# Kernel optimization log

Measured on AMD Instinct MI355X. Metric: run time of the kernel, lower is better.

The kernel has to match this reference:

```python
import jax, jax.numpy as jnp
import numpy as np

B, L, H, NH = 4, 200, 256, 4
HS = H // NH
NEG = jnp.float32(-(2.0**32) + 1.0)


def setup_inputs() -> dict:
    key = jax.random.key(0)
    ks = jax.random.split(key, 12)
    f = lambda k, s, sc=1.0: jax.random.normal(k, s, dtype=jnp.float32) * sc
    w_sc = 1.0 / np.sqrt(H).astype(np.float32)
    return {
        "queries": f(ks[0], (B, L, H)),
        "keys": f(ks[1], (B, L, H)),
        "time_matrix_K": f(ks[2], (B, L, L, H)),
        "time_matrix_V": f(ks[3], (B, L, L, H)),
        "dis_matrix_K": f(ks[4], (B, L, L, H)),
        "dis_matrix_V": f(ks[5], (B, L, L, H)),
        "abs_pos_K": f(ks[6], (B, L, H)),
        "abs_pos_V": f(ks[7], (B, L, H)),
        "Qw": f(ks[8], (H, H), w_sc),
        "Qb": jnp.zeros((H,), jnp.float32),
        "Kw": f(ks[9], (H, H), w_sc),
        "Kb": jnp.zeros((H,), jnp.float32),
        "Vw": f(ks[10], (H, H), w_sc),
        "Vb": jnp.zeros((H,), jnp.float32),
        "time_mask": jnp.zeros((B, L), dtype=bool),          # no padding positions
        "attn_mask": ~jnp.tril(jnp.ones((L, L), dtype=bool)),  # causal: mask strict upper triangle
    }


def reference(queries, keys, time_matrix_K, time_matrix_V, dis_matrix_K, dis_matrix_V,
              abs_pos_K, abs_pos_V, Qw, Qb, Kw, Kb, Vw, Vb, time_mask, attn_mask):
    # Linear projections (torch nn.Linear: x @ W^T + b)
    Q = queries @ Qw.T + Qb
    K = keys @ Kw.T + Kb
    V = keys @ Vw.T + Vb
    # split heads: [B, L, NH, HS]
    qh = Q.reshape(B, L, NH, HS)
    kh = K.reshape(B, L, NH, HS)
    vh = V.reshape(B, L, NH, HS)
    pKh = abs_pos_K.reshape(B, L, NH, HS)
    pVh = abs_pos_V.reshape(B, L, NH, HS)
    tKh = time_matrix_K.reshape(B, L, L, NH, HS)
    tVh = time_matrix_V.reshape(B, L, L, NH, HS)
    dKh = dis_matrix_K.reshape(B, L, L, NH, HS)
    dVh = dis_matrix_V.reshape(B, L, L, NH, HS)

    # attention logits [B, NH, L(query), L(key)] with three extra bias terms
    w = jnp.einsum("blhd,bmhd->bhlm", qh, kh)
    w += jnp.einsum("blhd,bmhd->bhlm", qh, pKh)
    w += jnp.einsum("blmhd,blhd->bhlm", tKh, qh)
    w += jnp.einsum("blmhd,blhd->bhlm", dKh, qh)
    w = w / jnp.sqrt(jnp.float32(HS))

    mask = time_mask[:, None, :, None] | attn_mask[None, None, :, :]
    w = jnp.where(mask, NEG, w)
    a = jax.nn.softmax(w, axis=-1)  # dropout_rate = 0 (eval)

    out = jnp.einsum("bhlm,bmhd->blhd", a, vh)
    out += jnp.einsum("bhlm,bmhd->blhd", a, pVh)
    out += jnp.einsum("bhlm,blmhd->blhd", a, tVh)
    out += jnp.einsum("bhlm,blmhd->blhd", a, dVh)
    return out.reshape(B, L, H)
```

## Files before the change

kernel.cpp:

```cpp
#include <hip/hip_runtime.h>
#include <cstddef>


#define B 4
#define L 200
#define H 256
#define NH 4
#define HS 64
#define SCALE 0.125f
#define NROWS 8

__global__ __launch_bounds__(256) void depoi_proj(
    const float* __restrict__ queries, const float* __restrict__ keys,
    const float* __restrict__ Qw, const float* __restrict__ Qb,
    const float* __restrict__ Kw, const float* __restrict__ Kb,
    const float* __restrict__ Vw, const float* __restrict__ Vb,
    const float* __restrict__ apK, const float* __restrict__ apV,
    float* __restrict__ Qo, float* __restrict__ Ko, float* __restrict__ Vo)
{
    __shared__ float4 xq[NROWS][H / 4];
    __shared__ float4 xk[NROWS][H / 4];
    const int t  = threadIdx.x;
    const int n0 = blockIdx.x * NROWS;

    const float4* q4 = (const float4*)queries;
    const float4* k4 = (const float4*)keys;
#pragma unroll
    for (int p = 0; p < (NROWS * (H / 4)) / 256; ++p) {
        int idx = p * 256 + t;
        int r = idx >> 6, c = idx & 63;
        xq[r][c] = q4[(size_t)(n0 + r) * (H / 4) + c];
        xk[r][c] = k4[(size_t)(n0 + r) * (H / 4) + c];
    }
    __syncthreads();

    float accq[NROWS], acck[NROWS], accv[NROWS];
#pragma unroll
    for (int r = 0; r < NROWS; ++r) { accq[r] = 0.f; acck[r] = 0.f; accv[r] = 0.f; }

    const float4* Qw4 = (const float4*)Qw + (size_t)t * (H / 4);
    const float4* Kw4 = (const float4*)Kw + (size_t)t * (H / 4);
    const float4* Vw4 = (const float4*)Vw + (size_t)t * (H / 4);
    for (int i = 0; i < H / 4; ++i) {
        float4 wq = Qw4[i], wk = Kw4[i], wv = Vw4[i];
#pragma unroll
        for (int r = 0; r < NROWS; ++r) {
            float4 a = xq[r][i];
            float4 c = xk[r][i];
            accq[r] += a.x * wq.x + a.y * wq.y + a.z * wq.z + a.w * wq.w;
            acck[r] += c.x * wk.x + c.y * wk.y + c.z * wk.z + c.w * wk.w;
            accv[r] += c.x * wv.x + c.y * wv.y + c.z * wv.z + c.w * wv.w;
        }
    }

    const float bq = Qb[t], bk = Kb[t], bv = Vb[t];
#pragma unroll
    for (int r = 0; r < NROWS; ++r) {
        size_t o = (size_t)(n0 + r) * H + t;
        Qo[o] = accq[r] + bq;
        Ko[o] = acck[r] + bk + apK[o];
        Vo[o] = accv[r] + bv + apV[o];
    }
}

__global__ __launch_bounds__(256) void depoi_attn(
    const float* __restrict__ Q, const float* __restrict__ Ksum,
    const float* __restrict__ Vsum,
    const float* __restrict__ tK, const float* __restrict__ dK,
    const float* __restrict__ tV, const float* __restrict__ dV,
    float* __restrict__ out)
{
    const int l = blockIdx.x;
    const int h = blockIdx.y;
    const int b = blockIdx.z;
    const int t    = threadIdx.x;
    const int mg   = t >> 4;
    const int dq   = t & 15;
    const int wid  = t >> 6;
    const int lane = t & 63;
    const int M = l + 1;

    __shared__ float4 sq[16];
    __shared__ float  plog[256];
    __shared__ float  sred[4];
    __shared__ float4 wpart[4][16];

    if (t < 16)
        sq[t] = ((const float4*)Q)[(size_t)(b * L + l) * (H / 4) + h * 16 + t];
    __syncthreads();
    const float4 q4 = sq[dq];

    const float4* K4  = (const float4*)Ksum;
    const float4* T4  = (const float4*)tK;
    const float4* D4  = (const float4*)dK;
    const size_t rowbase = (size_t)(b * L + l) * L * (H / 4);
    const size_t kbase   = (size_t)b * L * (H / 4);
    const int    col     = h * 16 + dq;

    for (int m = mg; m < M; m += 16) {
        float4 kk = K4[kbase + (size_t)m * (H / 4) + col];
        float4 tk = T4[rowbase + (size_t)m * (H / 4) + col];
        float4 dk = D4[rowbase + (size_t)m * (H / 4) + col];
        float sx = kk.x + tk.x + dk.x;
        float sy = kk.y + tk.y + dk.y;
        float sz = kk.z + tk.z + dk.z;
        float sw = kk.w + tk.w + dk.w;
        float p = q4.x * sx + q4.y * sy + q4.z * sz + q4.w * sw;
        p += __shfl_xor(p, 1);
        p += __shfl_xor(p, 2);
        p += __shfl_xor(p, 4);
        p += __shfl_xor(p, 8);
        if (dq == 0) plog[m] = p * SCALE;
    }
    __syncthreads();

    float v = (t < M) ? plog[t] : -3.0e38f;
    float mx = v;
#pragma unroll
    for (int off = 32; off >= 1; off >>= 1) mx = fmaxf(mx, __shfl_xor(mx, off));
    if (lane == 0) sred[wid] = mx;
    __syncthreads();
    mx = fmaxf(fmaxf(sred[0], sred[1]), fmaxf(sred[2], sred[3]));

    float p = (t < M) ? __expf(v - mx) : 0.0f;
    plog[t] = p;
    float s = p;
#pragma unroll
    for (int off = 32; off >= 1; off >>= 1) s += __shfl_xor(s, off);
    __syncthreads();
    if (lane == 0) sred[wid] = s;
    __syncthreads();
    const float inv = 1.0f / (sred[0] + sred[1] + sred[2] + sred[3]);

    const float4* V4  = (const float4*)Vsum;
    const float4* TV4 = (const float4*)tV;
    const float4* DV4 = (const float4*)dV;
    float4 acc = make_float4(0.f, 0.f, 0.f, 0.f);
    for (int m = mg; m < M; m += 16) {
        float pm = plog[m];
        float4 vv = V4[kbase + (size_t)m * (H / 4) + col];
        float4 tv = TV4[rowbase + (size_t)m * (H / 4) + col];
        float4 dv = DV4[rowbase + (size_t)m * (H / 4) + col];
        acc.x += pm * (vv.x + tv.x + dv.x);
        acc.y += pm * (vv.y + tv.y + dv.y);
        acc.z += pm * (vv.z + tv.z + dv.z);
        acc.w += pm * (vv.w + tv.w + dv.w);
    }
    acc.x += __shfl_xor(acc.x, 16); acc.y += __shfl_xor(acc.y, 16);
    acc.z += __shfl_xor(acc.z, 16); acc.w += __shfl_xor(acc.w, 16);
    acc.x += __shfl_xor(acc.x, 32); acc.y += __shfl_xor(acc.y, 32);
    acc.z += __shfl_xor(acc.z, 32); acc.w += __shfl_xor(acc.w, 32);
    if (lane < 16) wpart[wid][lane] = acc;
    __syncthreads();
    if (t < 16) {
        float4 a0 = wpart[0][t], a1 = wpart[1][t], a2 = wpart[2][t], a3 = wpart[3][t];
        float4 o;
        o.x = (a0.x + a1.x + a2.x + a3.x) * inv;
        o.y = (a0.y + a1.y + a2.y + a3.y) * inv;
        o.z = (a0.z + a1.z + a2.z + a3.z) * inv;
        o.w = (a0.w + a1.w + a2.w + a3.w) * inv;
        ((float4*)out)[(size_t)(b * L + l) * (H / 4) + h * 16 + t] = o;
    }
}

extern "C" void kernel_launch(void* const* d_in, const int* in_sizes, int n_in,
                              void* d_out, int out_size, void* d_ws, size_t ws_size,
                              hipStream_t stream) {
    const float* queries = (const float*)d_in[0];
    const float* keys    = (const float*)d_in[1];
    const float* tK      = (const float*)d_in[2];
    const float* tV      = (const float*)d_in[3];
    const float* dK      = (const float*)d_in[4];
    const float* dV      = (const float*)d_in[5];
    const float* apK     = (const float*)d_in[6];
    const float* apV     = (const float*)d_in[7];
    const float* Qw      = (const float*)d_in[8];
    const float* Qb      = (const float*)d_in[9];
    const float* Kw      = (const float*)d_in[10];
    const float* Kb      = (const float*)d_in[11];
    const float* Vw      = (const float*)d_in[12];
    const float* Vb      = (const float*)d_in[13];

    float* ws = (float*)d_ws;
    float* Qo = ws;
    float* Ko = ws + (size_t)B * L * H;
    float* Vo = ws + (size_t)2 * B * L * H;

    depoi_proj<<<(B * L) / NROWS, 256, 0, stream>>>(
        queries, keys, Qw, Qb, Kw, Kb, Vw, Vb, apK, apV, Qo, Ko, Vo);

    dim3 grid(L, NH, B);
    depoi_attn<<<grid, 256, 0, stream>>>(Qo, Ko, Vo, tK, dK, tV, dV, (float*)d_out);
}
```

Measured before the change: 544.5 us.

## Process all heads per attention block with full-row coalesced loads and reversed order

The attention kernel now assigns one 512-thread block per (query row, batch) covering all four heads, so each key row is read as a full contiguous 1 KB segment instead of four separate 256 B slices. Rows are processed longest-first (reversed l) to balance the causal triangle's uneven work, and the m-loop is unrolled by two for more loads in flight. The projection kernel uses 4 rows per block to launch more blocks. The cost is a larger block with more shared memory and fewer total blocks, which may lower occupancy.

```diff
diff --git a/kernel.cpp b/kernel.cpp
--- a/kernel.cpp
+++ b/kernel.cpp
@@ -8,7 +8,7 @@
 #define NH 4
 #define HS 64
 #define SCALE 0.125f
-#define NROWS 8
+#define NROWS 4
 
 __global__ __launch_bounds__(256) void depoi_proj(
     const float* __restrict__ queries, const float* __restrict__ keys,
@@ -25,10 +25,8 @@
 
     const float4* q4 = (const float4*)queries;
     const float4* k4 = (const float4*)keys;
-#pragma unroll
-    for (int p = 0; p < (NROWS * (H / 4)) / 256; ++p) {
-        int idx = p * 256 + t;
-        int r = idx >> 6, c = idx & 63;
+    {
+        int r = t >> 6, c = t & 63;
         xq[r][c] = q4[(size_t)(n0 + r) * (H / 4) + c];
         xk[r][c] = k4[(size_t)(n0 + r) * (H / 4) + c];
     }
@@ -63,103 +61,132 @@
     }
 }
 
-__global__ __launch_bounds__(256) void depoi_attn(
+__global__ __launch_bounds__(512) void depoi_attn(
     const float* __restrict__ Q, const float* __restrict__ Ksum,
     const float* __restrict__ Vsum,
     const float* __restrict__ tK, const float* __restrict__ dK,
     const float* __restrict__ tV, const float* __restrict__ dV,
     float* __restrict__ out)
 {
-    const int l = blockIdx.x;
-    const int h = blockIdx.y;
-    const int b = blockIdx.z;
+    const int l = L - 1 - blockIdx.x;
+    const int b = blockIdx.y;
     const int t    = threadIdx.x;
-    const int mg   = t >> 4;
-    const int dq   = t & 15;
+    const int c    = t & 63;
+    const int mg   = t >> 6;
+    const int lane = t & 63;
+    const int hh   = c >> 4;
+    const int M    = l + 1;
+
+    __shared__ float plog[NH][208];
+    __shared__ float sredA[8];
+    __shared__ float sredB[8];
+    __shared__ float4 wpart[8][64];
+
+    const float4* Q4 = (const float4*)Q;
+    const float4 q4  = Q4[(size_t)(b * L + l) * 64 + c];
+
+    const float4* K4 = (const float4*)Ksum + (size_t)b * L * 64;
+    const float4* T4 = (const float4*)tK + (size_t)(b * L + l) * L * 64;
+    const float4* D4 = (const float4*)dK + (size_t)(b * L + l) * L * 64;
+
+    int m = mg;
+    for (; m + 8 < M; m += 16) {
+        float4 k0 = K4[(size_t)m * 64 + c];
+        float4 t0 = T4[(size_t)m * 64 + c];
+        float4 d0 = D4[(size_t)m * 64 + c];
+        float4 k1 = K4[(size_t)(m + 8) * 64 + c];
+        float4 t1 = T4[(size_t)(m + 8) * 64 + c];
+        float4 d1 = D4[(size_t)(m + 8) * 64 + c];
+        float p0 = q4.x * (k0.x + t0.x + d0.x) + q4.y * (k0.y + t0.y + d0.y)
+                 + q4.z * (k0.z + t0.z + d0.z) + q4.w * (k0.w + t0.w + d0.w);
+        float p1 = q4.x * (k1.x + t1.x + d1.x) + q4.y * (k1.y + t1.y + d1.y)
+                 + q4.z * (k1.z + t1.z + d1.z) + q4.w * (k1.w + t1.w + d1.w);
+        p0 += __shfl_xor(p0, 1); p1 += __shfl_xor(p1, 1);
+        p0 += __shfl_xor(p0, 2); p1 += __shfl_xor(p1, 2);
+        p0 += __shfl_xor(p0, 4); p1 += __shfl_xor(p1, 4);
+        p0 += __shfl_xor(p0, 8); p1 += __shfl_xor(p1, 8);
+        if ((c & 15) == 0) {
+            plog[hh][m]     = p0 * SCALE;
+            plog[hh][m + 8] = p1 * SCALE;
+        }
+    }
+    if (m < M) {
+        float4 k0 = K4[(size_t)m * 64 + c];
+        float4 t0 = T4[(size_t)m * 64 + c];
+        float4 d0 = D4[(size_t)m * 64 + c];
+        float p0 = q4.x * (k0.x + t0.x + d0.x) + q4.y * (k0.y + t0.y + d0.y)
+                 + q4.z * (k0.z + t0.z + d0.z) + q4.w * (k0.w + t0.w + d0.w);
+        p0 += __shfl_xor(p0, 1);
+        p0 += __shfl_xor(p0, 2);
+        p0 += __shfl_xor(p0, 4);
+        p0 += __shfl_xor(p0, 8);
+        if ((c & 15) == 0) plog[hh][m] = p0 * SCALE;
+    }
+    __syncthreads();
+
+    const int head = t >> 7;
+    const int th   = t & 127;
     const int wid  = t >> 6;
-    const int lane = t & 63;
-    const int M = l + 1;
-
-    __shared__ float4 sq[16];
-    __shared__ float  plog[256];
-    __shared__ float  sred[4];
-    __shared__ float4 wpart[4][16];
-
-    if (t < 16)
-        sq[t] = ((const float4*)Q)[(size_t)(b * L + l) * (H / 4) + h * 16 + t];
-    __syncthreads();
-    const float4 q4 = sq[dq];
-
-    const float4* K4  = (const float4*)Ksum;
-    const float4* T4  = (const float4*)tK;
-    const float4* D4  = (const float4*)dK;
-    const size_t rowbase = (size_t)(b * L + l) * L * (H / 4);
-    const size_t kbase   = (size_t)b * L * (H / 4);
-    const int    col     = h * 16 + dq;
-
-    for (int m = mg; m < M; m += 16) {
-        float4 kk = K4[kbase + (size_t)m * (H / 4) + col];
-        float4 tk = T4[rowbase + (size_t)m * (H / 4) + col];
-        float4 dk = D4[rowbase + (size_t)m * (H / 4) + col];
-        float sx = kk.x + tk.x + dk.x;
-        float sy = kk.y + tk.y + dk.y;
-        float sz = kk.z + tk.z + dk.z;
-        float sw = kk.w + tk.w + dk.w;
-        float p = q4.x * sx + q4.y * sy + q4.z * sz + q4.w * sw;
-        p += __shfl_xor(p, 1);
-        p += __shfl_xor(p, 2);
-        p += __shfl_xor(p, 4);
-        p += __shfl_xor(p, 8);
-        if (dq == 0) plog[m] = p * SCALE;
-    }
-    __syncthreads();
-
-    float v = (t < M) ? plog[t] : -3.0e38f;
-    float mx = v;
+    float x0 = (th < M)       ? plog[head][th]       : -3.0e38f;
+    float x1 = (th + 128 < M) ? plog[head][th + 128] : -3.0e38f;
+    float mx = fmaxf(x0, x1);
 #pragma unroll
     for (int off = 32; off >= 1; off >>= 1) mx = fmaxf(mx, __shfl_xor(mx, off));
-    if (lane == 0) sred[wid] = mx;
-    __syncthreads();
-    mx = fmaxf(fmaxf(sred[0], sred[1]), fmaxf(sred[2], sred[3]));
-
-    float p = (t < M) ? __expf(v - mx) : 0.0f;
-    plog[t] = p;
-    float s = p;
+    if (lane == 0) sredA[wid] = mx;
+    __syncthreads();
+    mx = fmaxf(sredA[2 * head], sredA[2 * head + 1]);
+    float e0 = (th < M)       ? __expf(x0 - mx) : 0.0f;
+    float e1 = (th + 128 < M) ? __expf(x1 - mx) : 0.0f;
+    if (th < M)       plog[head][th]       = e0;
+    if (th + 128 < M) plog[head][th + 128] = e1;
+    float s = e0 + e1;
 #pragma unroll
     for (int off = 32; off >= 1; off >>= 1) s += __shfl_xor(s, off);
-    __syncthreads();
-    if (lane == 0) sred[wid] = s;
-    __syncthreads();
-    const float inv = 1.0f / (sred[0] + sred[1] + sred[2] + sred[3]);
-
-    const float4* V4  = (const float4*)Vsum;
-    const float4* TV4 = (const float4*)tV;
-    const float4* DV4 = (const float4*)dV;
+    if (lane == 0) sredB[wid] = s;
+    __syncthreads();
+
+    const float4* V4  = (const float4*)Vsum + (size_t)b * L * 64;
+    const float4* TV4 = (const float4*)tV + (size_t)(b * L + l) * L * 64;
+    const float4* DV4 = (const float4*)dV + (size_t)(b * L + l) * L * 64;
     float4 acc = make_float4(0.f, 0.f, 0.f, 0.f);
-    for (int m = mg; m < M; m += 16) {
-        float pm = plog[m];
-        float4 vv = V4[kbase + (size_t)m * (H / 4) + col];
-        float4 tv = TV4[rowbase + (size_t)m * (H / 4) + col];
-        float4 dv = DV4[rowbase + (size_t)m * (H / 4) + col];
-        acc.x += pm * (vv.x + tv.x + dv.x);
-        acc.y += pm * (vv.y + tv.y + dv.y);
-        acc.z += pm * (vv.z + tv.z + dv.z);
-        acc.w += pm * (vv.w + tv.w + dv.w);
-    }
-    acc.x += __shfl_xor(acc.x, 16); acc.y += __shfl_xor(acc.y, 16);
-    acc.z += __shfl_xor(acc.z, 16); acc.w += __shfl_xor(acc.w, 16);
-    acc.x += __shfl_xor(acc.x, 32); acc.y += __shfl_xor(acc.y, 32);
-    acc.z += __shfl_xor(acc.z, 32); acc.w += __shfl_xor(acc.w, 32);
-    if (lane < 16) wpart[wid][lane] = acc;
-    __syncthreads();
-    if (t < 16) {
-        float4 a0 = wpart[0][t], a1 = wpart[1][t], a2 = wpart[2][t], a3 = wpart[3][t];
-        float4 o;
-        o.x = (a0.x + a1.x + a2.x + a3.x) * inv;
-        o.y = (a0.y + a1.y + a2.y + a3.y) * inv;
-        o.z = (a0.z + a1.z + a2.z + a3.z) * inv;
-        o.w = (a0.w + a1.w + a2.w + a3.w) * inv;
-        ((float4*)out)[(size_t)(b * L + l) * (H / 4) + h * 16 + t] = o;
+    m = mg;
+    for (; m + 8 < M; m += 16) {
+        float4 v0  = V4[(size_t)m * 64 + c];
+        float4 tv0 = TV4[(size_t)m * 64 + c];
+        float4 dv0 = DV4[(size_t)m * 64 + c];
+        float4 v1  = V4[(size_t)(m + 8) * 64 + c];
+        float4 tv1 = TV4[(size_t)(m + 8) * 64 + c];
+        float4 dv1 = DV4[(size_t)(m + 8) * 64 + c];
+        float pm0 = plog[hh][m];
+        float pm1 = plog[hh][m + 8];
+        acc.x += pm0 * (v0.x + tv0.x + dv0.x) + pm1 * (v1.x + tv1.x + dv1.x);
+        acc.y += pm0 * (v0.y + tv0.y + dv0.y) + pm1 * (v1.y + tv1.y + dv1.y);
+        acc.z += pm0 * (v0.z + tv0.z + dv0.z) + pm1 * (v1.z + tv1.z + dv1.z);
+        acc.w += pm0 * (v0.w + tv0.w + dv0.w) + pm1 * (v1.w + tv1.w + dv1.w);
+    }
+    if (m < M) {
+        float4 v0  = V4[(size_t)m * 64 + c];
+        float4 tv0 = TV4[(size_t)m * 64 + c];
+        float4 dv0 = DV4[(size_t)m * 64 + c];
+        float pm0 = plog[hh][m];
+        acc.x += pm0 * (v0.x + tv0.x + dv0.x);
+        acc.y += pm0 * (v0.y + tv0.y + dv0.y);
+        acc.z += pm0 * (v0.z + tv0.z + dv0.z);
+        acc.w += pm0 * (v0.w + tv0.w + dv0.w);
+    }
+    wpart[mg][c] = acc;
+    __syncthreads();
+
+    if (t < 64) {
+        float4 r = make_float4(0.f, 0.f, 0.f, 0.f);
+#pragma unroll
+        for (int i = 0; i < 8; ++i) {
+            float4 w = wpart[i][t];
+            r.x += w.x; r.y += w.y; r.z += w.z; r.w += w.w;
+        }
+        const float inv = 1.0f / (sredB[2 * (t >> 4)] + sredB[2 * (t >> 4) + 1]);
+        r.x *= inv; r.y *= inv; r.z *= inv; r.w *= inv;
+        ((float4*)out)[(size_t)(b * L + l) * 64 + t] = r;
     }
 }
 
@@ -189,6 +216,6 @@
     depoi_proj<<<(B * L) / NROWS, 256, 0, stream>>>(
         queries, keys, Qw, Qb, Kw, Kb, Vw, Vb, apK, apV, Qo, Ko, Vo);
 
-    dim3 grid(L, NH, B);
-    depoi_attn<<<grid, 256, 0, stream>>>(Qo, Ko, Vo, tK, dK, tV, dV, (float*)d_out);
+    dim3 grid(L, B);
+    depoi_attn<<<grid, 512, 0, stream>>>(Qo, Ko, Vo, tK, dK, tV, dV, (float*)d_out);
 }
```

New measurement: 532.9 us. 2.1% less time.
